# Performance work log

Measured on AMD Instinct MI355X. Metric: run time of the kernel, lower is better.

## Reference

```python
import jax, jax.numpy as jnp
import numpy as np

# Dimensions
B, NIN, P, K, D, F = 8, 4096, 1024, 16, 2, 64
CPF, C, DM = 64, 128, 2
CIN = CPF + F
BN_EPS = 1e-3  # Keras BatchNormalization default epsilon


def _bn(x, prm):
    # inference-mode batchnorm; prm is (4, C): gamma, beta, moving_mean, moving_var
    g, b, m, v = prm
    return g * (x - m) * jax.lax.rsqrt(v + BN_EPS) + b


def setup_inputs() -> dict:
    key = jax.random.key(0)
    ks = jax.random.split(key, 24)
    s = 0.05
    def rn(k, shape):
        return jax.random.normal(k, shape, jnp.float32) * s
    def bn_prm(k, c):
        kg, kb, km, kv = jax.random.split(k, 4)
        return jnp.stack([
            1.0 + 0.1 * jax.random.normal(kg, (c,), jnp.float32),
            0.1 * jax.random.normal(kb, (c,), jnp.float32),
            0.1 * jax.random.normal(km, (c,), jnp.float32),
            jax.random.uniform(kv, (c,), jnp.float32, 0.5, 1.5),
        ])
    inputs = jax.random.normal(ks[0], (B, NIN, 3 + F), jnp.float32)
    return {
        "inputs": inputs,
        "W_pf1": rn(ks[1], (3, CPF)), "b_pf1": rn(ks[2], (CPF,)), "bn_pf1": bn_prm(ks[3], CPF),
        "W_pf2": rn(ks[4], (CPF, CPF)), "b_pf2": rn(ks[5], (CPF,)), "bn_pf2": bn_prm(ks[6], CPF),
        "W_c1": rn(ks[7], (K, 3, K * K)), "b_c1": rn(ks[8], (K * K,)), "bn_c1": bn_prm(ks[9], K * K),
        "W_c2": rn(ks[10], (K, K, K)), "b_c2": rn(ks[11], (K * K,)), "bn_c2": bn_prm(ks[12], K * K),
        "W_c3": rn(ks[13], (K, K, K)), "b_c3": rn(ks[14], (K * K,)), "bn_c3": bn_prm(ks[15], K * K),
        "W_df": rn(ks[16], (K, CIN, DM)), "W_pw": rn(ks[17], (CIN * DM, C)),
        "b_f": rn(ks[18], (C,)), "bn_f": bn_prm(ks[19], C),
    }


def reference(inputs, W_pf1, b_pf1, bn_pf1, W_pf2, b_pf2, bn_pf2,
              W_c1, b_c1, bn_c1, W_c2, b_c2, bn_c2, W_c3, b_c3, bn_c3,
              W_df, W_pw, b_f, bn_f):
    p = inputs[:, :, :3]              # (B, NIN, 3) positions
    q = p[:, :P, :]                   # (B, P, 3) 'random' sampled query points
    # knn_indices_general(q, p, K*D, sorted=True): squared-distance top-k
    d2 = (q * q).sum(-1)[:, :, None] + (p * p).sum(-1)[:, None, :] \
         - 2.0 * jnp.einsum('bqc,bpc->bqp', q, p)          # (B, P, NIN)
    _, idx_kd = jax.lax.top_k(-d2, K * D)                  # ascending distance
    idx = idx_kd[:, :, ::D]                                # dilation -> (B, P, K)
    gathered = jnp.take_along_axis(
        inputs, idx.reshape(B, P * K)[:, :, None], axis=1).reshape(B, P, K, 3 + F)
    p_nb = gathered[..., :3] - q[:, :, None, :]            # (B, P, K, 3) local coords
    f_nb = gathered[..., 3:]                               # (B, P, K, F)
    # pos -> feature: Dense, BN, Dense, BN (no activation in source)
    h = _bn(p_nb @ W_pf1 + b_pf1, bn_pf1)
    h = _bn(h @ W_pf2 + b_pf2, bn_pf2)
    feat = jnp.concatenate([h, f_nb], axis=-1)             # (B, P, K, CIN)
    # Conv2D(K*K, (1,K), elu) + BN: contraction over neighbor axis
    x = _bn(jax.nn.elu(jnp.einsum('bnjc,jco->bno', p_nb, W_c1) + b_c1), bn_c1)
    x = x.reshape(B, P, K, K)
    # DepthwiseConv2D((1,K), mult=K, elu) + BN; Keras channel order c*mult+m
    x = _bn(jax.nn.elu(jnp.einsum('bnwc,wcm->bncm', x, W_c2).reshape(B, P, K * K) + b_c2), bn_c2)
    x = x.reshape(B, P, K, K)
    x = _bn(jax.nn.elu(jnp.einsum('bnwc,wcm->bncm', x, W_c3).reshape(B, P, K * K) + b_c3), bn_c3)
    x = x.reshape(B, P, K, K)
    # per-point KxK X-transform on gathered features
    feat = jnp.einsum('bnij,bnjc->bnic', x, feat)          # (B, P, K, CIN)
    # SeparableConv2D(C, (1,K), mult=DM, elu) + BN; width axis collapses
    dw = jnp.einsum('bnjc,jcm->bncm', feat, W_df).reshape(B, P, CIN * DM)
    out = _bn(jax.nn.elu(dw @ W_pw + b_f), bn_f)           # (B, P, C)
    return jnp.concatenate([q, out], axis=-1)              # (B, P, 3 + C)
```

## Files before the change

### kernel.cpp

```cpp
#include <hip/hip_runtime.h>
#include <math.h>

#define B_    8
#define NIN_  4096
#define P_    1024
#define K_    16
#define F_    64
#define CH_   67
#define CPF_  64
#define CIN_  128
#define C_    128

#define S_PF1  0
#define SH_PF1 64
#define S_PF2  128
#define SH_PF2 192
#define S_C1   256
#define SH_C1  512
#define S_C2   768
#define SH_C2  1024
#define S_C3   1280
#define SH_C3  1536
#define S_F    1792
#define SH_F   1920
#define M_OFF  2048
#define C0_OFF 2240

#define WS_PTS_OFF  16384
#define WS_DWL_OFF  (WS_PTS_OFF + B_ * NIN_ * 16)

typedef float f2 __attribute__((ext_vector_type(2)));
typedef float f4 __attribute__((ext_vector_type(4)));

__device__ __forceinline__ float rlf(float x, int l) {
    return __int_as_float(__builtin_amdgcn_readlane(__float_as_int(x), l));
}
__device__ __forceinline__ int rli(int x, int l) {
    return __builtin_amdgcn_readlane(x, l);
}
__device__ __forceinline__ float eluf(float z) {
    return z > 0.f ? z : (__expf(z) - 1.0f);
}
__device__ __forceinline__ float dpp_shr1_ninf(float x) {
    return __int_as_float(__builtin_amdgcn_update_dpp(
        (int)0xFF800000, __float_as_int(x), 0x138, 0xF, 0xF, false));
}
__device__ __forceinline__ int dpp_shr1_i(int x) {
    return __builtin_amdgcn_update_dpp(x, x, 0x138, 0xF, 0xF, false);
}

__global__ __launch_bounds__(256) void prep_kernel(
    const float* __restrict__ inp, float4* __restrict__ pts,
    const float* __restrict__ bn_pf1, const float* __restrict__ bn_pf2,
    const float* __restrict__ bn_c1,  const float* __restrict__ bn_c2,
    const float* __restrict__ bn_c3,  const float* __restrict__ bn_f,
    const float* __restrict__ Wpf1,   const float* __restrict__ bpf1,
    const float* __restrict__ Wpf2,   const float* __restrict__ bpf2,
    float* __restrict__ wsf) {
    const int tid = threadIdx.x;
    if (blockIdx.x < 128) {
        int i = blockIdx.x * 256 + tid;
        const float* r = inp + (size_t)i * CH_;
        float x = r[0], y = r[1], z = r[2];
        float pp = __fadd_rn(__fadd_rn(__fmul_rn(x, x), __fmul_rn(y, y)),
                             __fmul_rn(z, z));
        pts[i] = make_float4(x, y, z, pp);
        return;
    }
#pragma unroll
    for (int it = 0; it < 4; ++it) {
        int t = it * 256 + tid;
        const float* src; int nch, c, so, sho;
        if (t < 64)       { src = bn_pf1; nch = 64;  c = t;        so = S_PF1; sho = SH_PF1; }
        else if (t < 128) { src = bn_pf2; nch = 64;  c = t - 64;   so = S_PF2; sho = SH_PF2; }
        else if (t < 384) { src = bn_c1;  nch = 256; c = t - 128;  so = S_C1;  sho = SH_C1; }
        else if (t < 640) { src = bn_c2;  nch = 256; c = t - 384;  so = S_C2;  sho = SH_C2; }
        else if (t < 896) { src = bn_c3;  nch = 256; c = t - 640;  so = S_C3;  sho = SH_C3; }
        else              { src = bn_f;   nch = 128; c = t - 896;  so = S_F;   sho = SH_F;  }
        float g = src[c], b = src[nch + c], m = src[2 * nch + c], v = src[3 * nch + c];
        float s = g * rsqrtf(v + 1e-3f);
        wsf[so + c]  = s;
        wsf[sho + c] = b - m * s;
    }
    __syncthreads();
    if (tid < 64) {
        int o = tid;
        float s2 = wsf[S_PF2 + o], t2 = wsf[SH_PF2 + o];
        float m0 = 0.f, m1 = 0.f, m2 = 0.f, cc = 0.f;
        for (int c = 0; c < 64; ++c) {
            float s1 = wsf[S_PF1 + c], t1 = wsf[SH_PF1 + c];
            float d1 = s1 * bpf1[c] + t1;
            float w2 = Wpf2[c * 64 + o];
            m0 += Wpf1[0 * 64 + c] * s1 * w2;
            m1 += Wpf1[1 * 64 + c] * s1 * w2;
            m2 += Wpf1[2 * 64 + c] * s1 * w2;
            cc += d1 * w2;
        }
        wsf[M_OFF + 0 * 64 + o] = m0 * s2;
        wsf[M_OFF + 1 * 64 + o] = m1 * s2;
        wsf[M_OFF + 2 * 64 + o] = m2 * s2;
        wsf[C0_OFF + o]         = cc * s2 + bpf2[o] * s2 + t2;
    }
}

__global__ __launch_bounds__(256) void fused_kernel(
    const float4* __restrict__ pts, const float* __restrict__ inp,
    const float* __restrict__ Wc1,  const float* __restrict__ bc1,
    const float* __restrict__ Wc2,  const float* __restrict__ bc2,
    const float* __restrict__ Wc3,  const float* __restrict__ bc3,
    const float* __restrict__ Wdf,  const float* __restrict__ wsf,
    float* __restrict__ dwl, float* __restrict__ out) {

    __shared__ float xA[4][256];
    __shared__ float xB[4][256];

    const int w   = threadIdx.x >> 6;
    const int l   = threadIdx.x & 63;
    const int wid = (blockIdx.x << 2) | w;
    const int b   = wid >> 10;
    const int qi  = wid & 1023;
    const float4* bp = pts + ((size_t)b << 12);

    const float4 q = bp[qi];
    const float qq = q.w;

#define DIST2(P) __fsub_rn(__fadd_rn(qq, (P).w), __fmul_rn(2.0f, \
    __fadd_rn(__fadd_rn(__fmul_rn(q.x, (P).x), __fmul_rn(q.y, (P).y)), \
              __fmul_rn(q.z, (P).z))))

    float4 p  = bp[l];
    float4 g1 = bp[64 + l];
    float4 g2 = bp[128 + l];
    float4 g3 = bp[192 + l];

    float d = DIST2(p);
    int ii = l;
#pragma unroll
    for (int k = 2; k <= 64; k <<= 1) {
#pragma unroll
        for (int j = k >> 1; j > 0; j >>= 1) {
            float od = __shfl_xor(d, j);
            int   oi = __shfl_xor(ii, j);
            bool keepmin = (((l & k) == 0) == ((l & j) == 0));
            bool ol = (od < d) || (od == d && oi < ii);
            bool take = keepmin ? ol : !ol;
            if (take) { d = od; ii = oi; }
        }
    }
    float bd = d;
    int   bi = ii;
    float kth = rlf(bd, 31);

#define INS_LOOP(MV, D2V, BASE)                                        \
    if (MV) {                                                          \
        do {                                                           \
            int c = (int)__builtin_ctzll(MV); MV &= MV - 1;            \
            float dc = rlf(D2V, c);                                    \
            int   ic = (BASE) + c;                                     \
            float prev  = dpp_shr1_ninf(bd);                           \
            int   previ = dpp_shr1_i(bi);                              \
            bool c1 = (bd > dc);                                       \
            bool c2 = (prev > dc);                                     \
            bd = fminf(bd, fmaxf(prev, dc));                           \
            bi = c1 ? (c2 ? previ : ic) : bi;                          \
        } while (MV);                                                  \
        kth = rlf(bd, 31);                                             \
    }

    {
        float d2 = DIST2(g1);
        unsigned long long m = __ballot(d2 < kth);
        INS_LOOP(m, d2, 64);
    }
    for (int j0 = 128; j0 < NIN_; j0 += 128) {
        float4 pa = g2, pb = g3;
        int jn = j0 + 128;
        if (jn < NIN_) { g2 = bp[jn + l]; g3 = bp[jn + 64 + l]; }
        float d2a = DIST2(pa);
        unsigned long long ma = __ballot(d2a < kth);
        INS_LOOP(ma, d2a, j0);
        float d2b = DIST2(pb);
        unsigned long long mb = __ballot(d2b < kth);
        INS_LOOP(mb, d2b, j0 + 64);
    }
#undef INS_LOOP
#undef DIST2

    const float* brow = inp + (size_t)b * NIN_ * CH_;
    const float q0 = q.x, q1 = q.y, q2 = q.z;

    float pd;
    {
        int k3 = (l * 21846) >> 16;
        k3 = (k3 > 15) ? 15 : k3;
        int d3 = l - ((k3 << 1) + k3);
        d3 = (d3 > 2) ? 2 : d3;
        int nbl = __shfl(bi, k3 << 1);
        float v = 0.f;
        if (l < 48) v = brow[(size_t)nbl * CH_ + d3];
        float qv = (d3 == 0) ? q0 : ((d3 == 1) ? q1 : q2);
        pd = v - qv;
    }

    {
        f4 acc = *reinterpret_cast<const f4*>(bc1 + 4 * l);
#pragma unroll 4
        for (int t4 = 0; t4 < 12; ++t4) {
            const float* wb = Wc1 + (size_t)(t4 * 4) * 256 + 4 * l;
            f4 w0 = *reinterpret_cast<const f4*>(wb);
            f4 w1 = *reinterpret_cast<const f4*>(wb + 256);
            f4 w2 = *reinterpret_cast<const f4*>(wb + 512);
            f4 w3 = *reinterpret_cast<const f4*>(wb + 768);
            float p0 = rlf(pd, 4 * t4 + 0);
            float p1 = rlf(pd, 4 * t4 + 1);
            float p2 = rlf(pd, 4 * t4 + 2);
            float p3 = rlf(pd, 4 * t4 + 3);
            acc += p0 * w0 + p1 * w1 + p2 * w2 + p3 * w3;
        }
        f4 sc = *reinterpret_cast<const f4*>(wsf + S_C1 + 4 * l);
        f4 sh = *reinterpret_cast<const f4*>(wsf + SH_C1 + 4 * l);
        f4 r;
        r.x = sc.x * eluf(acc.x) + sh.x;
        r.y = sc.y * eluf(acc.y) + sh.y;
        r.z = sc.z * eluf(acc.z) + sh.z;
        r.w = sc.w * eluf(acc.w) + sh.w;
        *reinterpret_cast<f4*>(&xA[w][4 * l]) = r;
    }

    {
        f4 acc = *reinterpret_cast<const f4*>(bc2 + 4 * l);
        const int csel = l >> 2;
#pragma unroll 8
        for (int w16 = 0; w16 < 16; ++w16) {
            float xs = xA[w][w16 * 16 + csel];
            f4 w4 = *reinterpret_cast<const f4*>(Wc2 + (size_t)w16 * 256 + 4 * l);
            acc += xs * w4;
        }
        f4 sc = *reinterpret_cast<const f4*>(wsf + S_C2 + 4 * l);
        f4 sh = *reinterpret_cast<const f4*>(wsf + SH_C2 + 4 * l);
        f4 r;
        r.x = sc.x * eluf(acc.x) + sh.x;
        r.y = sc.y * eluf(acc.y) + sh.y;
        r.z = sc.z * eluf(acc.z) + sh.z;
        r.w = sc.w * eluf(acc.w) + sh.w;
        *reinterpret_cast<f4*>(&xB[w][4 * l]) = r;
    }

    {
        f4 acc = *reinterpret_cast<const f4*>(bc3 + 4 * l);
        const int csel = l >> 2;
#pragma unroll 8
        for (int w16 = 0; w16 < 16; ++w16) {
            float xs = xB[w][w16 * 16 + csel];
            f4 w4 = *reinterpret_cast<const f4*>(Wc3 + (size_t)w16 * 256 + 4 * l);
            acc += xs * w4;
        }
        f4 sc = *reinterpret_cast<const f4*>(wsf + S_C3 + 4 * l);
        f4 sh = *reinterpret_cast<const f4*>(wsf + SH_C3 + 4 * l);
        f4 r;
        r.x = sc.x * eluf(acc.x) + sh.x;
        r.y = sc.y * eluf(acc.y) + sh.y;
        r.z = sc.z * eluf(acc.z) + sh.z;
        r.w = sc.w * eluf(acc.w) + sh.w;
        *reinterpret_cast<f4*>(&xA[w][4 * l]) = r;
    }

    f2 hf[16];
    {
        const float Mw0 = wsf[M_OFF + l];
        const float Mw1 = wsf[M_OFF + 64 + l];
        const float Mw2 = wsf[M_OFF + 128 + l];
        const float cc0 = wsf[C0_OFF + l];
#pragma unroll
        for (int k = 0; k < 16; ++k) {
            int nbs = rli(bi, 2 * k);
            float fv = brow[(size_t)nbs * CH_ + 3 + l];
            float s0 = rlf(pd, 3 * k), s1 = rlf(pd, 3 * k + 1), s2 = rlf(pd, 3 * k + 2);
            float hv = fmaf(s0, Mw0, fmaf(s1, Mw1, fmaf(s2, Mw2, cc0)));
            f2 t; t.x = hv; t.y = fv;
            hf[k] = t;
        }
    }

    f2 dlo; dlo.x = 0.f; dlo.y = 0.f;
    f2 dhi = dlo;
#pragma unroll 4
    for (int i = 0; i < 16; ++i) {
        const f4* xr = reinterpret_cast<const f4*>(&xA[w][i * 16]);
        f4 x0 = xr[0], x1 = xr[1], x2 = xr[2], x3v = xr[3];
        f2 fab = x0.x * hf[0]  + x0.y * hf[1]  + x0.z * hf[2]  + x0.w * hf[3]
               + x1.x * hf[4]  + x1.y * hf[5]  + x1.z * hf[6]  + x1.w * hf[7]
               + x2.x * hf[8]  + x2.y * hf[9]  + x2.z * hf[10] + x2.w * hf[11]
               + x3v.x * hf[12]+ x3v.y * hf[13]+ x3v.z * hf[14]+ x3v.w * hf[15];
        const float* wr = Wdf + (size_t)i * 256;
        f2 wlo = *reinterpret_cast<const f2*>(wr + 2 * l);
        f2 whi = *reinterpret_cast<const f2*>(wr + 128 + 2 * l);
        dlo += fab.x * wlo;
        dhi += fab.y * whi;
    }
    float* drow = dwl + (size_t)wid * 256;
    *reinterpret_cast<f2*>(drow + 2 * l)       = dlo;
    *reinterpret_cast<f2*>(drow + 128 + 2 * l) = dhi;

    if (l < 3) out[(size_t)wid * 131 + l] = (l == 0) ? q0 : ((l == 1) ? q1 : q2);
}

__global__ __launch_bounds__(256) void pw_kernel(const float* __restrict__ dwl,
                                                 const float* __restrict__ Wpw,
                                                 const float* __restrict__ bf,
                                                 const float* __restrict__ wsf,
                                                 float* __restrict__ out) {
    __shared__ float As[32][256];
    const int tid = threadIdx.x;
    const int m0  = blockIdx.x * 32;

#pragma unroll
    for (int i = 0; i < 8; ++i) {
        int fi  = i * 1024 + tid * 4;
        int row = fi >> 8, col = fi & 255;
        *reinterpret_cast<float4*>(&As[row][col]) =
            *reinterpret_cast<const float4*>(dwl + (size_t)(m0 + row) * 256 + col);
    }
    __syncthreads();

    const int mq = tid >> 5;
    const int nq = tid & 31;
    f4 acc[4];
#pragma unroll
    for (int mi = 0; mi < 4; ++mi) { acc[mi].x = 0.f; acc[mi].y = 0.f; acc[mi].z = 0.f; acc[mi].w = 0.f; }

#pragma unroll 4
    for (int k4 = 0; k4 < 64; ++k4) {
        f4 a[4], bw[4];
#pragma unroll
        for (int mi = 0; mi < 4; ++mi)
            a[mi] = *reinterpret_cast<const f4*>(&As[mq * 4 + mi][k4 * 4]);
#pragma unroll
        for (int ki = 0; ki < 4; ++ki)
            bw[ki] = *reinterpret_cast<const f4*>(Wpw + (size_t)(k4 * 4 + ki) * 128 + nq * 4);
#pragma unroll
        for (int mi = 0; mi < 4; ++mi) {
            acc[mi] += a[mi].x * bw[0] + a[mi].y * bw[1] + a[mi].z * bw[2] + a[mi].w * bw[3];
        }
    }

    f4 b4  = *reinterpret_cast<const f4*>(bf + nq * 4);
    f4 sc4 = *reinterpret_cast<const f4*>(wsf + S_F + nq * 4);
    f4 sh4 = *reinterpret_cast<const f4*>(wsf + SH_F + nq * 4);
#pragma unroll
    for (int mi = 0; mi < 4; ++mi) {
        const int m = m0 + mq * 4 + mi;
        float* orow = out + (size_t)m * 131 + 3 + nq * 4;
        orow[0] = sc4.x * eluf(acc[mi].x + b4.x) + sh4.x;
        orow[1] = sc4.y * eluf(acc[mi].y + b4.y) + sh4.y;
        orow[2] = sc4.z * eluf(acc[mi].z + b4.z) + sh4.z;
        orow[3] = sc4.w * eluf(acc[mi].w + b4.w) + sh4.w;
    }
}

extern "C" void kernel_launch(void* const* d_in, const int* in_sizes, int n_in,
                              void* d_out, int out_size, void* d_ws, size_t ws_size,
                              hipStream_t stream) {
    const float* inp   = (const float*)d_in[0];
    const float* Wpf1  = (const float*)d_in[1];
    const float* bpf1  = (const float*)d_in[2];
    const float* bnpf1 = (const float*)d_in[3];
    const float* Wpf2  = (const float*)d_in[4];
    const float* bpf2  = (const float*)d_in[5];
    const float* bnpf2 = (const float*)d_in[6];
    const float* Wc1   = (const float*)d_in[7];
    const float* bc1   = (const float*)d_in[8];
    const float* bnc1  = (const float*)d_in[9];
    const float* Wc2   = (const float*)d_in[10];
    const float* bc2   = (const float*)d_in[11];
    const float* bnc2  = (const float*)d_in[12];
    const float* Wc3   = (const float*)d_in[13];
    const float* bc3   = (const float*)d_in[14];
    const float* bnc3  = (const float*)d_in[15];
    const float* Wdf   = (const float*)d_in[16];
    const float* Wpw   = (const float*)d_in[17];
    const float* bf    = (const float*)d_in[18];
    const float* bnf   = (const float*)d_in[19];

    float*  wsf  = (float*)d_ws;
    float4* pts  = (float4*)((char*)d_ws + WS_PTS_OFF);
    float*  dwl  = (float*)((char*)d_ws + WS_DWL_OFF);
    float*  outp = (float*)d_out;

    hipLaunchKernelGGL(prep_kernel, dim3(129), dim3(256), 0, stream,
                       inp, pts, bnpf1, bnpf2, bnc1, bnc2, bnc3, bnf,
                       Wpf1, bpf1, Wpf2, bpf2, wsf);
    hipLaunchKernelGGL(fused_kernel, dim3((B_ * P_) / 4), dim3(256), 0, stream,
                       pts, inp, Wc1, bc1, Wc2, bc2, Wc3, bc3, Wdf, wsf,
                       dwl, outp);
    hipLaunchKernelGGL(pw_kernel, dim3((B_ * P_) / 32), dim3(256), 0, stream,
                       dwl, Wpw, bf, wsf, outp);
}
```

Baseline: 105.8 us.

## Halve distance scaling, split prep reduction across warps, shrink pw_kernel tile

Three unrelated changes. Point norms are stored pre-halved so the distance computation drops a multiply by two, which preserves the neighbour ordering up to rounding. The prep kernel's 64-channel weight fold is now split across all four waves and combined through shared memory, so it is no longer done serially by one wave. The pointwise GEMM tile goes from 32 to 16 rows, doubling the block count for better occupancy at the cost of more repeated reads of Wpw.

```diff
diff --git a/kernel.cpp b/kernel.cpp
--- a/kernel.cpp
+++ b/kernel.cpp
@@ -64,7 +64,7 @@
         float x = r[0], y = r[1], z = r[2];
         float pp = __fadd_rn(__fadd_rn(__fmul_rn(x, x), __fmul_rn(y, y)),
                              __fmul_rn(z, z));
-        pts[i] = make_float4(x, y, z, pp);
+        pts[i] = make_float4(x, y, z, __fmul_rn(0.5f, pp));
         return;
     }
 #pragma unroll
@@ -83,11 +83,11 @@
         wsf[sho + c] = b - m * s;
     }
     __syncthreads();
-    if (tid < 64) {
-        int o = tid;
-        float s2 = wsf[S_PF2 + o], t2 = wsf[SH_PF2 + o];
+    {
+        __shared__ float4 red[4][64];
+        const int o = tid & 63, part = tid >> 6;
         float m0 = 0.f, m1 = 0.f, m2 = 0.f, cc = 0.f;
-        for (int c = 0; c < 64; ++c) {
+        for (int c = part * 16; c < part * 16 + 16; ++c) {
             float s1 = wsf[S_PF1 + c], t1 = wsf[SH_PF1 + c];
             float d1 = s1 * bpf1[c] + t1;
             float w2 = Wpf2[c * 64 + o];
@@ -96,10 +96,20 @@
             m2 += Wpf1[2 * 64 + c] * s1 * w2;
             cc += d1 * w2;
         }
-        wsf[M_OFF + 0 * 64 + o] = m0 * s2;
-        wsf[M_OFF + 1 * 64 + o] = m1 * s2;
-        wsf[M_OFF + 2 * 64 + o] = m2 * s2;
-        wsf[C0_OFF + o]         = cc * s2 + bpf2[o] * s2 + t2;
+        red[part][o] = make_float4(m0, m1, m2, cc);
+        __syncthreads();
+        if (part == 0) {
+            float4 p0 = red[0][o], p1 = red[1][o], p2 = red[2][o], p3 = red[3][o];
+            float M0 = ((p0.x + p1.x) + p2.x) + p3.x;
+            float M1 = ((p0.y + p1.y) + p2.y) + p3.y;
+            float M2 = ((p0.z + p1.z) + p2.z) + p3.z;
+            float CC = ((p0.w + p1.w) + p2.w) + p3.w;
+            float s2 = wsf[S_PF2 + o], t2 = wsf[SH_PF2 + o];
+            wsf[M_OFF + 0 * 64 + o] = M0 * s2;
+            wsf[M_OFF + 1 * 64 + o] = M1 * s2;
+            wsf[M_OFF + 2 * 64 + o] = M2 * s2;
+            wsf[C0_OFF + o]         = CC * s2 + bpf2[o] * s2 + t2;
+        }
     }
 }
 
@@ -122,11 +132,11 @@
     const float4* bp = pts + ((size_t)b << 12);
 
     const float4 q = bp[qi];
-    const float qq = q.w;
-
-#define DIST2(P) __fsub_rn(__fadd_rn(qq, (P).w), __fmul_rn(2.0f, \
+    const float hq = q.w;
+
+#define DIST2(P) __fsub_rn(__fadd_rn(hq, (P).w), \
     __fadd_rn(__fadd_rn(__fmul_rn(q.x, (P).x), __fmul_rn(q.y, (P).y)), \
-              __fmul_rn(q.z, (P).z))))
+              __fmul_rn(q.z, (P).z)))
 
     float4 p  = bp[l];
     float4 g1 = bp[64 + l];
@@ -310,12 +320,12 @@
                                                  const float* __restrict__ bf,
                                                  const float* __restrict__ wsf,
                                                  float* __restrict__ out) {
-    __shared__ float As[32][256];
+    __shared__ float As[16][256];
     const int tid = threadIdx.x;
-    const int m0  = blockIdx.x * 32;
-
-#pragma unroll
-    for (int i = 0; i < 8; ++i) {
+    const int m0  = blockIdx.x * 16;
+
+#pragma unroll
+    for (int i = 0; i < 4; ++i) {
         int fi  = i * 1024 + tid * 4;
         int row = fi >> 8, col = fi & 255;
         *reinterpret_cast<float4*>(&As[row][col]) =
@@ -325,21 +335,21 @@
 
     const int mq = tid >> 5;
     const int nq = tid & 31;
-    f4 acc[4];
-#pragma unroll
-    for (int mi = 0; mi < 4; ++mi) { acc[mi].x = 0.f; acc[mi].y = 0.f; acc[mi].z = 0.f; acc[mi].w = 0.f; }
+    f4 acc[2];
+#pragma unroll
+    for (int mi = 0; mi < 2; ++mi) { acc[mi].x = 0.f; acc[mi].y = 0.f; acc[mi].z = 0.f; acc[mi].w = 0.f; }
 
 #pragma unroll 4
     for (int k4 = 0; k4 < 64; ++k4) {
-        f4 a[4], bw[4];
-#pragma unroll
-        for (int mi = 0; mi < 4; ++mi)
-            a[mi] = *reinterpret_cast<const f4*>(&As[mq * 4 + mi][k4 * 4]);
+        f4 a[2], bw[4];
+#pragma unroll
+        for (int mi = 0; mi < 2; ++mi)
+            a[mi] = *reinterpret_cast<const f4*>(&As[mq * 2 + mi][k4 * 4]);
 #pragma unroll
         for (int ki = 0; ki < 4; ++ki)
             bw[ki] = *reinterpret_cast<const f4*>(Wpw + (size_t)(k4 * 4 + ki) * 128 + nq * 4);
 #pragma unroll
-        for (int mi = 0; mi < 4; ++mi) {
+        for (int mi = 0; mi < 2; ++mi) {
             acc[mi] += a[mi].x * bw[0] + a[mi].y * bw[1] + a[mi].z * bw[2] + a[mi].w * bw[3];
         }
     }
@@ -348,8 +358,8 @@
     f4 sc4 = *reinterpret_cast<const f4*>(wsf + S_F + nq * 4);
     f4 sh4 = *reinterpret_cast<const f4*>(wsf + SH_F + nq * 4);
 #pragma unroll
-    for (int mi = 0; mi < 4; ++mi) {
-        const int m = m0 + mq * 4 + mi;
+    for (int mi = 0; mi < 2; ++mi) {
+        const int m = m0 + mq * 2 + mi;
         float* orow = out + (size_t)m * 131 + 3 + nq * 4;
         orow[0] = sc4.x * eluf(acc[mi].x + b4.x) + sh4.x;
         orow[1] = sc4.y * eluf(acc[mi].y + b4.y) + sh4.y;
@@ -393,6 +403,6 @@
     hipLaunchKernelGGL(fused_kernel, dim3((B_ * P_) / 4), dim3(256), 0, stream,
                        pts, inp, Wc1, bc1, Wc2, bc2, Wc3, bc3, Wdf, wsf,
                        dwl, outp);
-    hipLaunchKernelGGL(pw_kernel, dim3((B_ * P_) / 32), dim3(256), 0, stream,
+    hipLaunchKernelGGL(pw_kernel, dim3((B_ * P_) / 16), dim3(256), 0, stream,
                        dwl, Wpw, bf, wsf, outp);
 }
```

Result: no change. 107.0 us (+1.2%).
